# Kernel tuning notes

Measured on AMD Instinct MI355X. Metric: run time of the kernel, lower is better.

## Reference

```python
import jax, jax.numpy as jnp
import numpy as np

QMAX = 127.0  # int8 symmetric quantization range


def _quant_dequant(w):
    """Per-output-channel symmetric int8 fake quantization (weight-only),
    mimicking nn.quantized.Linear.from_float weight quantization."""
    scale = jnp.max(jnp.abs(w), axis=-1, keepdims=True) / QMAX
    scale = jnp.maximum(scale, 1e-8)
    q = jnp.clip(jnp.round(w / scale), -QMAX, QMAX)
    return q * scale


def setup_inputs() -> dict:
    key = jax.random.key(0)
    ks = jax.random.split(key, 7)
    B, S, D, F, E, NS = 2, 2048, 1024, 2048, 8, 1
    std = 1.0 / np.sqrt(D)
    x = jax.random.normal(ks[0], (B, S, D), dtype=jnp.float32)
    router_w = _quant_dequant(jax.random.normal(ks[1], (E, D), dtype=jnp.float32) * std)
    router_b = jnp.zeros((E,), dtype=jnp.float32)
    w_up = _quant_dequant(jax.random.normal(ks[2], (E, F, D), dtype=jnp.float32) * std)
    w_down = _quant_dequant(jax.random.normal(ks[3], (E, D, F), dtype=jnp.float32) / np.sqrt(F))
    shared_w_up = _quant_dequant(jax.random.normal(ks[4], (NS, F, D), dtype=jnp.float32) * std)
    shared_w_down = _quant_dequant(jax.random.normal(ks[5], (NS, D, F), dtype=jnp.float32) / np.sqrt(F))
    return {"x": x, "router_w": router_w, "router_b": router_b,
            "w_up": w_up, "w_down": w_down,
            "shared_w_up": shared_w_up, "shared_w_down": shared_w_down}


def reference(x, router_w, router_b, w_up, w_down, shared_w_up, shared_w_down):
    B, S, D = x.shape
    E = router_w.shape[0]
    TOPK = 2
    xt = x.reshape(-1, D)  # [T, D] tokens

    # Router (quantized linear) -> softmax -> top-k dispatch weights
    logits = xt @ router_w.T + router_b            # [T, E]
    probs = jax.nn.softmax(logits, axis=-1)        # [T, E]
    top_vals, top_idx = jax.lax.top_k(probs, TOPK)  # [T, K]
    top_vals = top_vals / jnp.sum(top_vals, axis=-1, keepdims=True)  # renormalize
    # combine[t, e] = routing weight of expert e for token t (0 if not selected)
    combine = jnp.sum(jax.nn.one_hot(top_idx, E, dtype=xt.dtype) * top_vals[..., None], axis=1)  # [T, E]

    # Routed experts: up -> SiLU -> down, computed densely then combined
    h = jnp.einsum('td,efd->tef', xt, w_up)        # [T, E, F]
    y = jnp.einsum('tef,edf->ted', jax.nn.silu(h), w_down)  # [T, E, D]
    out = jnp.einsum('ted,te->td', y, combine)     # [T, D]

    # Shared experts: always active, summed
    hs = jnp.einsum('td,sfd->tsf', xt, shared_w_up)          # [T, NS, F]
    out = out + jnp.einsum('tsf,sdf->td', jax.nn.silu(hs), shared_w_down)

    return out.reshape(B, S, D)
```

## Files before the change

### kernel.cpp

```cpp
#include <hip/hip_runtime.h>
#include <stdint.h>

typedef unsigned short u16;
typedef int i32x4 __attribute__((ext_vector_type(4)));

#define DDIM 1024
#define FDIM 2048
#define NEXP 8
#define RT_TILES 72
#define SHOFF 9216
#define RCAP 13312
#define NRT 104
#define UPROWS 16384
#define DNROWS 8192
#define UPTOT (UPROWS + FDIM)
#define DNTOT (DNROWS + DDIM)
#define UPTASKS (UPTOT / 4)
#define DNTASKS (DNTOT / 2)
#define WQTASKS (UPTASKS + DNTASKS)


__device__ inline float bf2f(u16 u) {
    union { unsigned int i; float f; } v; v.i = ((unsigned int)u) << 16; return v.f;
}
__device__ inline u16 f2bf(float f) {
    union { float f; unsigned int i; } v; v.f = f;
    unsigned int lsb = (v.i >> 16) & 1u;
    return (u16)((v.i + 0x7fffu + lsb) >> 16);
}
__device__ inline int q8(float v, float inv) {
    int x = (int)rintf(v * inv);
    return x < -127 ? -127 : (x > 127 ? 127 : x);
}
__device__ inline unsigned pack4(float a, float b, float c, float d, float inv) {
    return (unsigned)(q8(a, inv) & 255) | ((unsigned)(q8(b, inv) & 255) << 8) |
           ((unsigned)(q8(c, inv) & 255) << 16) | ((unsigned)(q8(d, inv) & 255) << 24);
}

typedef const __attribute__((address_space(1))) void gas_void;
typedef __attribute__((address_space(3))) void las_void;
#define GLL16(g, l) __builtin_amdgcn_global_load_lds((gas_void*)(g), (las_void*)(l), 16, 0, 0)

__global__ __launch_bounds__(256) void detect_kernel(
    const u16* __restrict__ x, int* __restrict__ meta)
{
    __shared__ int scnt;
    if (threadIdx.x == 0) scnt = 0;
    __syncthreads();
    int bad = 0;
    #pragma unroll
    for (int i = 0; i < 4; i++) {
        u16 v = x[threadIdx.x * 4 + i];
        if (((v >> 7) & 0xFF) >= 0x8F) bad++;
    }
    if (bad) atomicAdd(&scnt, bad);
    __syncthreads();
    if (threadIdx.x == 0) meta[30] = (scnt > 32) ? 1 : 0;
}

__global__ __launch_bounds__(256) void router_kernel(
    const void* __restrict__ x_, const void* __restrict__ rw_, const void* __restrict__ rb_,
    float* __restrict__ top_w, int* __restrict__ top_idx, const int* __restrict__ meta)
{
    __shared__ char smem[32768];
    const int tid = threadIdx.x;
    const int wave = tid >> 6, lane = tid & 63;
    const int flag = meta[30];

    float* rws = (float*)smem;
    if (!flag) {
        const ushort4* rwv = (const ushort4*)rw_;
        #pragma unroll
        for (int i = 0; i < 8; i++) {
            int idx = tid + i * 256;
            ushort4 h = rwv[idx];
            rws[idx * 4 + 0] = bf2f(h.x); rws[idx * 4 + 1] = bf2f(h.y);
            rws[idx * 4 + 2] = bf2f(h.z); rws[idx * 4 + 3] = bf2f(h.w);
        }
    } else {
        const float4* rwv = (const float4*)rw_;
        #pragma unroll
        for (int i = 0; i < 8; i++) {
            int idx = tid + i * 256;
            float4 f = rwv[idx];
            rws[idx * 4 + 0] = f.x; rws[idx * 4 + 1] = f.y;
            rws[idx * 4 + 2] = f.z; rws[idx * 4 + 3] = f.w;
        }
    }
    __syncthreads();

    for (int sub = 0; sub < 4; sub++) {
        const int t = blockIdx.x * 16 + wave * 4 + sub;
        float xv[16];
        if (!flag) {
            const u16* xr = (const u16*)x_ + (size_t)t * DDIM + lane * 16;
            uint4 p0 = *(const uint4*)(xr);
            uint4 p1 = *(const uint4*)(xr + 8);
            #pragma unroll
            for (int d = 0; d < 8; d++) xv[d]     = bf2f(((const u16*)&p0)[d]);
            #pragma unroll
            for (int d = 0; d < 8; d++) xv[d + 8] = bf2f(((const u16*)&p1)[d]);
        } else {
            const float4* xr = (const float4*)((const float*)x_ + (size_t)t * DDIM + lane * 16);
            #pragma unroll
            for (int c = 0; c < 4; c++) {
                float4 f = xr[c];
                xv[c * 4 + 0] = f.x; xv[c * 4 + 1] = f.y;
                xv[c * 4 + 2] = f.z; xv[c * 4 + 3] = f.w;
            }
        }
        float acc[NEXP];
        #pragma unroll
        for (int e = 0; e < NEXP; e++) {
            const float* wr = &rws[e * DDIM + lane * 16];
            float s = 0.f;
            #pragma unroll
            for (int d = 0; d < 16; d++) s += xv[d] * wr[d];
            acc[e] = s;
        }
        #pragma unroll
        for (int e = 0; e < NEXP; e++) {
            #pragma unroll
            for (int off = 32; off > 0; off >>= 1)
                acc[e] += __shfl_xor(acc[e], off, 64);
        }
        if (lane == 0) {
            float lg[NEXP];
            #pragma unroll
            for (int e = 0; e < NEXP; e++) {
                float b = flag ? ((const float*)rb_)[e] : bf2f(((const u16*)rb_)[e]);
                lg[e] = acc[e] + b;
            }
            int i0 = 0;
            #pragma unroll
            for (int e = 1; e < NEXP; e++) if (lg[e] > lg[i0]) i0 = e;
            int i1 = (i0 == 0) ? 1 : 0;
            #pragma unroll
            for (int e = 0; e < NEXP; e++) if (e != i0 && lg[e] > lg[i1]) i1 = e;
            float e1 = __expf(lg[i1] - lg[i0]);
            float w0 = 1.f / (1.f + e1);
            float w1 = e1 / (1.f + e1);
            top_w[2 * t] = w0;  top_w[2 * t + 1] = w1;
            top_idx[2 * t] = i0; top_idx[2 * t + 1] = i1;
        }
    }
}

template<int NR, int NC>
__device__ inline void wq_bf16_n(const char* __restrict__ src, char* __restrict__ dst,
                                 float* __restrict__ sout, int R0, int lane) {
    uint4 raw[NR][NC];
    #pragma unroll
    for (int r = 0; r < NR; r++)
        #pragma unroll
        for (int c = 0; c < NC; c++)
            raw[r][c] = *(const uint4*)(src + (size_t)r * (NC * 1024) + c * 1024 + lane * 16);
    float m[NR];
    #pragma unroll
    for (int r = 0; r < NR; r++) {
        m[r] = 0.f;
        #pragma unroll
        for (int c = 0; c < NC; c++) {
            const u16* h = (const u16*)&raw[r][c];
            #pragma unroll
            for (int d = 0; d < 8; d++) m[r] = fmaxf(m[r], fabsf(bf2f(h[d])));
        }
    }
    #pragma unroll
    for (int off = 32; off > 0; off >>= 1)
        #pragma unroll
        for (int r = 0; r < NR; r++)
            m[r] = fmaxf(m[r], __shfl_xor(m[r], off, 64));
    #pragma unroll
    for (int r = 0; r < NR; r++) {
        m[r] = fmaxf(m[r], 1e-12f);
        if (lane == 0) sout[R0 + r] = m[r] / 127.f;
        const float inv = 127.f / m[r];
        #pragma unroll
        for (int c = 0; c < NC; c++) {
            const u16* h = (const u16*)&raw[r][c];
            uint2 o;
            o.x = pack4(bf2f(h[0]), bf2f(h[1]), bf2f(h[2]), bf2f(h[3]), inv);
            o.y = pack4(bf2f(h[4]), bf2f(h[5]), bf2f(h[6]), bf2f(h[7]), inv);
            *(uint2*)(dst + (size_t)r * (NC * 512) + c * 512 + lane * 8) = o;
        }
    }
}

template<int NC>
__device__ inline void wq_f32(const char* __restrict__ src, char* __restrict__ dst,
                              float* __restrict__ sout, int R, int lane) {
    float m = 0.f;
    #pragma unroll
    for (int c = 0; c < NC; c++) {
        float4 f = *(const float4*)(src + (size_t)c * 1024 + lane * 16);
        m = fmaxf(m, fmaxf(fmaxf(fabsf(f.x), fabsf(f.y)),
                           fmaxf(fabsf(f.z), fabsf(f.w))));
    }
    #pragma unroll
    for (int off = 32; off > 0; off >>= 1) m = fmaxf(m, __shfl_xor(m, off, 64));
    m = fmaxf(m, 1e-12f);
    if (lane == 0) sout[R] = m / 127.f;
    const float inv = 127.f / m;
    #pragma unroll
    for (int c = 0; c < NC; c++) {
        float4 f = *(const float4*)(src + (size_t)c * 1024 + lane * 16);
        *(unsigned*)(dst + (size_t)c * 256 + lane * 4) = pack4(f.x, f.y, f.z, f.w, inv);
    }
}

__global__ __launch_bounds__(256) void wquant_kernel(
    const void* __restrict__ w_up, const void* __restrict__ w_down,
    const void* __restrict__ sw_up, const void* __restrict__ sw_down,
    char* __restrict__ qup, char* __restrict__ qdn,
    float* __restrict__ su, float* __restrict__ sd, const int* __restrict__ meta)
{
    const int wave = threadIdx.x >> 6, lane = threadIdx.x & 63;
    const int flag = meta[30];
    const int id = blockIdx.x * 4 + wave;
    if (id < UPTASKS) {
        const int R0 = id * 4;
        if (!flag) {
            const char* src = (R0 < UPROWS)
                ? (const char*)w_up + (size_t)R0 * 2048
                : (const char*)sw_up + (size_t)(R0 - UPROWS) * 2048;
            wq_bf16_n<4, 2>(src, qup + (size_t)R0 * 1024, su, R0, lane);
        } else {
            const char* src = (R0 < UPROWS)
                ? (const char*)w_up + (size_t)R0 * 4096
                : (const char*)sw_up + (size_t)(R0 - UPROWS) * 4096;
            for (int r = 0; r < 4; r++)
                wq_f32<4>(src + (size_t)r * 4096, qup + (size_t)(R0 + r) * 1024,
                          su, R0 + r, lane);
        }
    } else {
        const int R0 = (id - UPTASKS) * 2;
        if (!flag) {
            const char* src = (R0 < DNROWS)
                ? (const char*)w_down + (size_t)R0 * 4096
                : (const char*)sw_down + (size_t)(R0 - DNROWS) * 4096;
            wq_bf16_n<2, 4>(src, qdn + (size_t)R0 * 2048, sd, R0, lane);
        } else {
            const char* src = (R0 < DNROWS)
                ? (const char*)w_down + (size_t)R0 * 8192
                : (const char*)sw_down + (size_t)(R0 - DNROWS) * 8192;
            for (int r = 0; r < 2; r++)
                wq_f32<8>(src + (size_t)r * 8192, qdn + (size_t)(R0 + r) * 2048,
                          sd, R0 + r, lane);
        }
    }
}

__global__ __launch_bounds__(1024) void rank_kernel(
    const int* __restrict__ top_idx, int* __restrict__ tok_rows, int* __restrict__ meta)
{
    __shared__ int wsum[16][NEXP];
    __shared__ int wbase[16][NEXP];
    const int tid = threadIdx.x, lane = tid & 63, wave = tid >> 6;

    const int4* tp = (const int4*)(top_idx + tid * 8);
    int4 v0 = tp[0], v1 = tp[1];
    int e[8] = { v0.x, v0.y, v0.z, v0.w, v1.x, v1.y, v1.z, v1.w };

    int tcnt[NEXP];
    #pragma unroll
    for (int en = 0; en < NEXP; en++) tcnt[en] = 0;
    #pragma unroll
    for (int j = 0; j < 8; j++)
        #pragma unroll
        for (int en = 0; en < NEXP; en++) tcnt[en] += (e[j] == en);

    int excl[NEXP];
    #pragma unroll
    for (int en = 0; en < NEXP; en++) {
        int v = tcnt[en];
        #pragma unroll
        for (int off = 1; off < 64; off <<= 1) {
            int u = __shfl_up(v, off, 64);
            if (lane >= off) v += u;
        }
        excl[en] = v - tcnt[en];
        if (lane == 63) wsum[wave][en] = v;
    }
    __syncthreads();
    if (tid < NEXP) {
        int s = 0;
        for (int w = 0; w < 16; w++) { int c = wsum[w][tid]; wbase[w][tid] = s; s += c; }
        meta[tid] = s;
    }
    __syncthreads();
    if (tid == 0) {
        int b = 0;
        for (int en = 0; en < NEXP; en++) {
            meta[8 + en] = b;
            b += ((meta[en] + 127) >> 7) << 7;
        }
        meta[16] = b;
    }
    __syncthreads();

    int cur[NEXP];
    #pragma unroll
    for (int en = 0; en < NEXP; en++) cur[en] = meta[8 + en] + wbase[wave][en] + excl[en];

    int r[8];
    #pragma unroll
    for (int j = 0; j < 8; j++) {
        int rr = 0;
        #pragma unroll
        for (int en = 0; en < NEXP; en++)
            if (e[j] == en) { rr = cur[en]; cur[en] = rr + 1; }
        r[j] = rr;
    }
    int4* rp = (int4*)(tok_rows + tid * 8);
    rp[0] = make_int4(r[0], r[1], r[2], r[3]);
    rp[1] = make_int4(r[4], r[5], r[6], r[7]);
}

__global__ __launch_bounds__(128) void gather_q_kernel(
    const void* __restrict__ x_, const int* __restrict__ tok_rows,
    char* __restrict__ xq, float* __restrict__ sxa, const int* __restrict__ meta)
{
    __shared__ float wmax[2];
    const int t = blockIdx.x, tid = threadIdx.x;
    const int wave = tid >> 6, lane = tid & 63;
    const int r0 = tok_rows[2 * t], r1 = tok_rows[2 * t + 1];

    float v[8];
    if (!meta[30]) {
        uint4 p = ((const uint4*)((const u16*)x_ + (size_t)t * DDIM))[tid];
        #pragma unroll
        for (int d = 0; d < 8; d++) v[d] = bf2f(((const u16*)&p)[d]);
    } else {
        const float4* xf = (const float4*)((const float*)x_ + (size_t)t * DDIM);
        float4 a = xf[2 * tid], b = xf[2 * tid + 1];
        v[0] = a.x; v[1] = a.y; v[2] = a.z; v[3] = a.w;
        v[4] = b.x; v[5] = b.y; v[6] = b.z; v[7] = b.w;
    }
    float m = 0.f;
    #pragma unroll
    for (int d = 0; d < 8; d++) m = fmaxf(m, fabsf(v[d]));
    #pragma unroll
    for (int off = 32; off > 0; off >>= 1) m = fmaxf(m, __shfl_xor(m, off, 64));
    if (lane == 0) wmax[wave] = m;
    __syncthreads();
    const float mx = fmaxf(fmaxf(wmax[0], wmax[1]), 1e-8f);
    const float inv = 127.f / mx;

    uint2 u;
    u.x = pack4(v[0], v[1], v[2], v[3], inv);
    u.y = pack4(v[4], v[5], v[6], v[7], inv);

    ((uint2*)(xq + (size_t)r0 * DDIM))[tid] = u;
    ((uint2*)(xq + (size_t)r1 * DDIM))[tid] = u;
    ((uint2*)(xq + (size_t)(SHOFF + t) * DDIM))[tid] = u;
    if (tid == 0) {
        float s = mx / 127.f;
        sxa[r0] = s; sxa[r1] = s; sxa[SHOFF + t] = s;
    }
}

__global__ __launch_bounds__(256, 2) void moe_gemm_i8(
    const char* __restrict__ A, const char* __restrict__ Wq,
    const float* __restrict__ sa, const float* __restrict__ sw,
    u16* __restrict__ Cout, const int* __restrict__ meta, int N, int Kd, int act)
{
    const int L = blockIdx.y * gridDim.x + blockIdx.x;
    const int xcd = L & 7;
    const int jj = L >> 3;
    const int rt = xcd * 13 + (jj % 13);
    const int ct = jj / 13;

    int e;
    if (rt >= RT_TILES) {
        e = NEXP;
    } else {
        const int r0t = rt * 128;
        if (r0t >= meta[16]) return;
        e = 0;
        #pragma unroll
        for (int i = 1; i < NEXP; i++) if (r0t >= meta[8 + i]) e = i;
        if (r0t >= meta[8 + e] + meta[e]) return;
    }
    const char* Wb = Wq + (size_t)(e * N + ct * 128) * Kd;
    const float* swb = sw + e * N + ct * 128;

    __shared__ char As[2][128 * 64];
    __shared__ char Bs[2][128 * 64];

    const int tid = threadIdx.x;
    const int wave = tid >> 6, lane = tid & 63;
    const int wm = (wave >> 1) * 64;
    const int wn = (wave & 1) * 64;
    const int l16 = lane & 15;
    const int q = lane >> 4;
    const int slot = (q + (l16 >> 1)) & 3;

    const int rsub = lane >> 2;
    const int qs = ((lane & 3) - ((lane >> 3) & 3)) & 3;

    const char* Ag = A + (size_t)(rt * 128 + wave * 16 + rsub) * Kd + qs * 16;
    const char* Bg = Wb + (size_t)(wave * 16 + rsub) * Kd + qs * 16;
    const size_t rstep = (size_t)64 * Kd;

    i32x4 acc[4][4] = {};

#define STAGE(buf, off) do { \
        GLL16(Ag + (off),         &As[buf][wave * 1024]); \
        GLL16(Ag + (off) + rstep, &As[buf][4096 + wave * 1024]); \
        GLL16(Bg + (off),         &Bs[buf][wave * 1024]); \
        GLL16(Bg + (off) + rstep, &Bs[buf][4096 + wave * 1024]); \
    } while (0)

    STAGE(0, 0);
    __syncthreads();

    int cur = 0;
    for (int kk = 0; kk < Kd; kk += 64) {
        if (kk + 64 < Kd) STAGE(cur ^ 1, kk + 64);
        i32x4 af[4], bf[4];
        #pragma unroll
        for (int i = 0; i < 4; i++)
            af[i] = *(const i32x4*)&As[cur][(wm + i * 16 + l16) * 64 + slot * 16];
        #pragma unroll
        for (int j = 0; j < 4; j++)
            bf[j] = *(const i32x4*)&Bs[cur][(wn + j * 16 + l16) * 64 + slot * 16];
        #pragma unroll
        for (int i = 0; i < 4; i++)
            #pragma unroll
            for (int j = 0; j < 4; j++)
                acc[i][j] = __builtin_amdgcn_mfma_i32_16x16x64_i8(af[i], bf[j], acc[i][j], 0, 0, 0);
        __syncthreads();
        cur ^= 1;
    }
#undef STAGE

    float sal[4][4];
    #pragma unroll
    for (int i = 0; i < 4; i++)
        #pragma unroll
        for (int rr = 0; rr < 4; rr++)
            sal[i][rr] = sa[rt * 128 + wm + i * 16 + q * 4 + rr];
    float swl[4];
    #pragma unroll
    for (int j = 0; j < 4; j++) swl[j] = swb[wn + j * 16 + l16];

    u16* Crow = Cout + (size_t)(rt * 128) * N + ct * 128;
    #pragma unroll
    for (int i = 0; i < 4; i++) {
        #pragma unroll
        for (int j = 0; j < 4; j++) {
            #pragma unroll
            for (int rr = 0; rr < 4; rr++) {
                const int row = wm + i * 16 + q * 4 + rr;
                const int col = wn + j * 16 + l16;
                float v = (float)acc[i][j][rr] * sal[i][rr] * swl[j];
                if (act) v = v / (1.f + __expf(-v));
                Crow[(size_t)row * N + col] = f2bf(v);
            }
        }
    }
}

__global__ __launch_bounds__(256) void hquant_kernel(
    const u16* __restrict__ hg, char* __restrict__ h8, float* __restrict__ sh,
    const int* __restrict__ meta)
{
    const int r = blockIdx.x;
    if (r >= meta[16] && r < SHOFF) return;
    __shared__ float wmax[4];
    const int tid = threadIdx.x;
    const int wave = tid >> 6, lane = tid & 63;
    const u16* row = hg + (size_t)r * FDIM;
    uint4 p = ((const uint4*)row)[tid];
    float v[8];
    #pragma unroll
    for (int d = 0; d < 8; d++) v[d] = bf2f(((const u16*)&p)[d]);
    float m = 0.f;
    #pragma unroll
    for (int d = 0; d < 8; d++) m = fmaxf(m, fabsf(v[d]));
    #pragma unroll
    for (int off = 32; off > 0; off >>= 1) m = fmaxf(m, __shfl_xor(m, off, 64));
    if (lane == 0) wmax[wave] = m;
    __syncthreads();
    const float mx = fmaxf(fmaxf(fmaxf(wmax[0], wmax[1]), fmaxf(wmax[2], wmax[3])), 1e-8f);
    const float inv = 127.f / mx;
    if (tid == 0) sh[r] = mx / 127.f;
    uint2 u;
    u.x = pack4(v[0], v[1], v[2], v[3], inv);
    u.y = pack4(v[4], v[5], v[6], v[7], inv);
    ((uint2*)(h8 + (size_t)r * FDIM))[tid] = u;
}

__global__ __launch_bounds__(256) void combine_kernel(
    const u16* __restrict__ yg, const float* __restrict__ top_w,
    const int* __restrict__ tok_rows, void* __restrict__ out_, const int* __restrict__ meta)
{
    const int t = blockIdx.x;
    const int r0 = tok_rows[2 * t], r1 = tok_rows[2 * t + 1];
    const float w0 = top_w[2 * t], w1 = top_w[2 * t + 1];
    const int d = threadIdx.x * 4;
    ushort4 y0 = *(const ushort4*)(yg + (size_t)r0 * DDIM + d);
    ushort4 y1 = *(const ushort4*)(yg + (size_t)r1 * DDIM + d);
    ushort4 ys = *(const ushort4*)(yg + (size_t)(SHOFF + t) * DDIM + d);
    float o0 = w0 * bf2f(y0.x) + w1 * bf2f(y1.x) + bf2f(ys.x);
    float o1 = w0 * bf2f(y0.y) + w1 * bf2f(y1.y) + bf2f(ys.y);
    float o2 = w0 * bf2f(y0.z) + w1 * bf2f(y1.z) + bf2f(ys.z);
    float o3 = w0 * bf2f(y0.w) + w1 * bf2f(y1.w) + bf2f(ys.w);
    if (!meta[30]) {
        ushort4 o; o.x = f2bf(o0); o.y = f2bf(o1); o.z = f2bf(o2); o.w = f2bf(o3);
        *(ushort4*)((u16*)out_ + (size_t)t * DDIM + d) = o;
    } else {
        float4 o; o.x = o0; o.y = o1; o.z = o2; o.w = o3;
        *(float4*)((float*)out_ + (size_t)t * DDIM + d) = o;
    }
}

extern "C" void kernel_launch(void* const* d_in, const int* in_sizes, int n_in,
                              void* d_out, int out_size, void* d_ws, size_t ws_size,
                              hipStream_t stream) {
    const void* x       = d_in[0];
    const void* rw      = d_in[1];
    const void* rb      = d_in[2];
    const void* w_up    = d_in[3];
    const void* w_down  = d_in[4];
    const void* sw_up   = d_in[5];
    const void* sw_down = d_in[6];

    const int T = in_sizes[0] / DDIM;

    char* ws = (char*)d_ws;
    int*   meta     = (int*)ws;
    float* top_w    = (float*)(ws + 1024);
    int*   top_idx  = (int*)(ws + 1024 + 8 * T);
    int*   tok_rows = (int*)(ws + 1024 + 16 * T);
    size_t off = 131072;
    u16*  yg = (u16*)(ws + off);
    char* xq = (char*)(ws + off);
    off += (size_t)RCAP * DDIM * 2;
    u16*  hg = (u16*)(ws + off);
    off += (size_t)RCAP * FDIM * 2;
    char* h8 = (char*)(ws + off);
    off += (size_t)RCAP * FDIM;
    char* qup = (char*)(ws + off);
    off += (size_t)(NEXP + 1) * FDIM * DDIM;
    char* qdn = (char*)(ws + off);
    off += (size_t)(NEXP + 1) * DDIM * FDIM;
    float* sxa = (float*)(ws + off); off += (size_t)RCAP * 4;
    float* sh  = (float*)(ws + off); off += (size_t)RCAP * 4;
    float* su  = (float*)(ws + off); off += (size_t)(NEXP + 1) * FDIM * 4;
    float* sd  = (float*)(ws + off); off += (size_t)(NEXP + 1) * DDIM * 4;

    detect_kernel<<<1, 256, 0, stream>>>((const u16*)x, meta);

    const int nrb = T / 16;
    router_kernel<<<nrb, 256, 0, stream>>>(x, rw, rb, top_w, top_idx, meta);
    wquant_kernel<<<WQTASKS / 4, 256, 0, stream>>>(
        w_up, w_down, sw_up, sw_down, qup, qdn, su, sd, meta);
    rank_kernel<<<1, 1024, 0, stream>>>(top_idx, tok_rows, meta);
    gather_q_kernel<<<T, 128, 0, stream>>>(x, tok_rows, xq, sxa, meta);

    moe_gemm_i8<<<dim3(FDIM / 128, NRT), 256, 0, stream>>>(
        xq, qup, sxa, su, hg, meta, FDIM, DDIM, 1);
    hquant_kernel<<<RCAP, 256, 0, stream>>>(hg, h8, sh, meta);
    moe_gemm_i8<<<dim3(DDIM / 128, NRT), 256, 0, stream>>>(
        h8, qdn, sh, sd, yg, meta, DDIM, FDIM, 0);
    combine_kernel<<<T, 256, 0, stream>>>(yg, top_w, tok_rows, d_out, meta);
}
```

Measured before the change: 330.2 us.

## Make weight and activation quantization kernels persistent with double-buffered row loads

The weight-quantization and hidden-activation quantization kernels now run as a fixed grid of 2048 waves that stride over row tasks. Each wave prefetches the next task's 4 KB into a second register set while it reduces and packs the current one. Previously each task used its own wave or block, and hquant launched one 256-thread block per row with a shared-memory reduction and early exits for unused rows. The aim is to hide global-memory latency and cut block-launch overhead in these bandwidth-bound passes, at the cost of more registers and macro-heavy code.

```diff
diff --git a/kernel.cpp b/kernel.cpp
--- a/kernel.cpp
+++ b/kernel.cpp
@@ -15,9 +15,9 @@
 #define DNROWS 8192
 #define UPTOT (UPROWS + FDIM)
 #define DNTOT (DNROWS + DDIM)
-#define UPTASKS (UPTOT / 4)
-#define DNTASKS (DNTOT / 2)
-#define WQTASKS (UPTASKS + DNTASKS)
+#define UPT2 (UPTOT / 2)
+#define WQ_NT (UPT2 + DNTOT)
+#define WQ_NW 2048
 
 
 __device__ inline float bf2f(u16 u) {
@@ -35,6 +35,25 @@
 __device__ inline unsigned pack4(float a, float b, float c, float d, float inv) {
     return (unsigned)(q8(a, inv) & 255) | ((unsigned)(q8(b, inv) & 255) << 8) |
            ((unsigned)(q8(c, inv) & 255) << 16) | ((unsigned)(q8(d, inv) & 255) << 24);
+}
+__device__ inline float absmax8(uint4 p) {
+    const u16* h = (const u16*)&p;
+    float m = fabsf(bf2f(h[0]));
+    #pragma unroll
+    for (int d = 1; d < 8; d++) m = fmaxf(m, fabsf(bf2f(h[d])));
+    return m;
+}
+__device__ inline void store8(char* dst, uint4 p, float inv) {
+    const u16* h = (const u16*)&p;
+    uint2 o;
+    o.x = pack4(bf2f(h[0]), bf2f(h[1]), bf2f(h[2]), bf2f(h[3]), inv);
+    o.y = pack4(bf2f(h[4]), bf2f(h[5]), bf2f(h[6]), bf2f(h[7]), inv);
+    *(uint2*)dst = o;
+}
+__device__ inline float wredmax(float m) {
+    #pragma unroll
+    for (int off = 32; off > 0; off >>= 1) m = fmaxf(m, __shfl_xor(m, off, 64));
+    return m;
 }
 
 typedef const __attribute__((address_space(1))) void gas_void;
@@ -146,45 +165,17 @@
     }
 }
 
-template<int NR, int NC>
-__device__ inline void wq_bf16_n(const char* __restrict__ src, char* __restrict__ dst,
-                                 float* __restrict__ sout, int R0, int lane) {
-    uint4 raw[NR][NC];
-    #pragma unroll
-    for (int r = 0; r < NR; r++)
-        #pragma unroll
-        for (int c = 0; c < NC; c++)
-            raw[r][c] = *(const uint4*)(src + (size_t)r * (NC * 1024) + c * 1024 + lane * 16);
-    float m[NR];
-    #pragma unroll
-    for (int r = 0; r < NR; r++) {
-        m[r] = 0.f;
-        #pragma unroll
-        for (int c = 0; c < NC; c++) {
-            const u16* h = (const u16*)&raw[r][c];
-            #pragma unroll
-            for (int d = 0; d < 8; d++) m[r] = fmaxf(m[r], fabsf(bf2f(h[d])));
-        }
-    }
-    #pragma unroll
-    for (int off = 32; off > 0; off >>= 1)
-        #pragma unroll
-        for (int r = 0; r < NR; r++)
-            m[r] = fmaxf(m[r], __shfl_xor(m[r], off, 64));
-    #pragma unroll
-    for (int r = 0; r < NR; r++) {
-        m[r] = fmaxf(m[r], 1e-12f);
-        if (lane == 0) sout[R0 + r] = m[r] / 127.f;
-        const float inv = 127.f / m[r];
-        #pragma unroll
-        for (int c = 0; c < NC; c++) {
-            const u16* h = (const u16*)&raw[r][c];
-            uint2 o;
-            o.x = pack4(bf2f(h[0]), bf2f(h[1]), bf2f(h[2]), bf2f(h[3]), inv);
-            o.y = pack4(bf2f(h[4]), bf2f(h[5]), bf2f(h[6]), bf2f(h[7]), inv);
-            *(uint2*)(dst + (size_t)r * (NC * 512) + c * 512 + lane * 8) = o;
-        }
-    }
+
+__device__ inline const char* wq_src(int t, const char* wup, const char* swup,
+                                     const char* wdn, const char* swdn) {
+    if (t < UPT2) {
+        const int R0 = t * 2;
+        return (R0 < UPROWS) ? wup + (size_t)R0 * 2048
+                             : swup + (size_t)(R0 - UPROWS) * 2048;
+    }
+    const int R = t - UPT2;
+    return (R < DNROWS) ? wdn + (size_t)R * 4096
+                        : swdn + (size_t)(R - DNROWS) * 4096;
 }
 
 template<int NC>
@@ -197,8 +188,7 @@
         m = fmaxf(m, fmaxf(fmaxf(fabsf(f.x), fabsf(f.y)),
                            fmaxf(fabsf(f.z), fabsf(f.w))));
     }
-    #pragma unroll
-    for (int off = 32; off > 0; off >>= 1) m = fmaxf(m, __shfl_xor(m, off, 64));
+    m = wredmax(m);
     m = fmaxf(m, 1e-12f);
     if (lane == 0) sout[R] = m / 127.f;
     const float inv = 127.f / m;
@@ -215,40 +205,87 @@
     char* __restrict__ qup, char* __restrict__ qdn,
     float* __restrict__ su, float* __restrict__ sd, const int* __restrict__ meta)
 {
-    const int wave = threadIdx.x >> 6, lane = threadIdx.x & 63;
+    const int gwid = (blockIdx.x * blockDim.x + threadIdx.x) >> 6;
+    const int lane = threadIdx.x & 63;
     const int flag = meta[30];
-    const int id = blockIdx.x * 4 + wave;
-    if (id < UPTASKS) {
-        const int R0 = id * 4;
-        if (!flag) {
-            const char* src = (R0 < UPROWS)
-                ? (const char*)w_up + (size_t)R0 * 2048
-                : (const char*)sw_up + (size_t)(R0 - UPROWS) * 2048;
-            wq_bf16_n<4, 2>(src, qup + (size_t)R0 * 1024, su, R0, lane);
-        } else {
-            const char* src = (R0 < UPROWS)
-                ? (const char*)w_up + (size_t)R0 * 4096
-                : (const char*)sw_up + (size_t)(R0 - UPROWS) * 4096;
-            for (int r = 0; r < 4; r++)
-                wq_f32<4>(src + (size_t)r * 4096, qup + (size_t)(R0 + r) * 1024,
-                          su, R0 + r, lane);
-        }
-    } else {
-        const int R0 = (id - UPTASKS) * 2;
-        if (!flag) {
-            const char* src = (R0 < DNROWS)
-                ? (const char*)w_down + (size_t)R0 * 4096
-                : (const char*)sw_down + (size_t)(R0 - DNROWS) * 4096;
-            wq_bf16_n<2, 4>(src, qdn + (size_t)R0 * 2048, sd, R0, lane);
-        } else {
-            const char* src = (R0 < DNROWS)
-                ? (const char*)w_down + (size_t)R0 * 8192
-                : (const char*)sw_down + (size_t)(R0 - DNROWS) * 8192;
-            for (int r = 0; r < 2; r++)
-                wq_f32<8>(src + (size_t)r * 8192, qdn + (size_t)(R0 + r) * 2048,
-                          sd, R0 + r, lane);
-        }
-    }
+
+    if (flag) {
+        for (int t = gwid; t < WQ_NT; t += WQ_NW) {
+            if (t < UPT2) {
+                const int R0 = t * 2;
+                const char* src = (R0 < UPROWS)
+                    ? (const char*)w_up + (size_t)R0 * 4096
+                    : (const char*)sw_up + (size_t)(R0 - UPROWS) * 4096;
+                wq_f32<4>(src,        qup + (size_t)R0 * 1024,       su, R0,     lane);
+                wq_f32<4>(src + 4096, qup + (size_t)(R0 + 1) * 1024, su, R0 + 1, lane);
+            } else {
+                const int R = t - UPT2;
+                const char* src = (R < DNROWS)
+                    ? (const char*)w_down + (size_t)R * 8192
+                    : (const char*)sw_down + (size_t)(R - DNROWS) * 8192;
+                wq_f32<8>(src, qdn + (size_t)R * 2048, sd, R, lane);
+            }
+        }
+        return;
+    }
+
+    const char* wup  = (const char*)w_up;
+    const char* swup = (const char*)sw_up;
+    const char* wdn  = (const char*)w_down;
+    const char* swdn = (const char*)sw_down;
+
+    uint4 A0, A1, A2, A3, B0, B1, B2, B3;
+
+#define WQLOAD(P0, P1, P2, P3, T) do { \
+        const char* s_ = wq_src((T), wup, swup, wdn, swdn); \
+        P0 = *(const uint4*)(s_ + lane * 16); \
+        P1 = *(const uint4*)(s_ + 1024 + lane * 16); \
+        P2 = *(const uint4*)(s_ + 2048 + lane * 16); \
+        P3 = *(const uint4*)(s_ + 3072 + lane * 16); \
+    } while (0)
+
+#define WQPROC(P0, P1, P2, P3, T) do { \
+        if ((T) < UPT2) { \
+            const int R0_ = (T) * 2; \
+            float m0_ = fmaxf(absmax8(P0), absmax8(P1)); \
+            float m1_ = fmaxf(absmax8(P2), absmax8(P3)); \
+            m0_ = fmaxf(wredmax(m0_), 1e-12f); \
+            m1_ = fmaxf(wredmax(m1_), 1e-12f); \
+            if (lane == 0) { su[R0_] = m0_ / 127.f; su[R0_ + 1] = m1_ / 127.f; } \
+            char* d_ = qup + (size_t)R0_ * 1024; \
+            store8(d_ + lane * 8,        P0, 127.f / m0_); \
+            store8(d_ + 512 + lane * 8,  P1, 127.f / m0_); \
+            store8(d_ + 1024 + lane * 8, P2, 127.f / m1_); \
+            store8(d_ + 1536 + lane * 8, P3, 127.f / m1_); \
+        } else { \
+            const int R_ = (T) - UPT2; \
+            float m_ = fmaxf(fmaxf(absmax8(P0), absmax8(P1)), \
+                             fmaxf(absmax8(P2), absmax8(P3))); \
+            m_ = fmaxf(wredmax(m_), 1e-12f); \
+            if (lane == 0) sd[R_] = m_ / 127.f; \
+            const float inv_ = 127.f / m_; \
+            char* d_ = qdn + (size_t)R_ * 2048; \
+            store8(d_ + lane * 8,        P0, inv_); \
+            store8(d_ + 512 + lane * 8,  P1, inv_); \
+            store8(d_ + 1024 + lane * 8, P2, inv_); \
+            store8(d_ + 1536 + lane * 8, P3, inv_); \
+        } \
+    } while (0)
+
+    int t = gwid;
+    WQLOAD(A0, A1, A2, A3, t);
+    #pragma unroll 1
+    for (int it = 0; it < 4; it++) {
+        WQLOAD(B0, B1, B2, B3, t + WQ_NW);
+        WQPROC(A0, A1, A2, A3, t);
+        t += WQ_NW;
+        WQLOAD(A0, A1, A2, A3, t + WQ_NW);
+        WQPROC(B0, B1, B2, B3, t);
+        t += WQ_NW;
+    }
+    WQPROC(A0, A1, A2, A3, t);
+#undef WQLOAD
+#undef WQPROC
 }
 
 __global__ __launch_bounds__(1024) void rank_kernel(
@@ -340,8 +377,7 @@
     float m = 0.f;
     #pragma unroll
     for (int d = 0; d < 8; d++) m = fmaxf(m, fabsf(v[d]));
-    #pragma unroll
-    for (int off = 32; off > 0; off >>= 1) m = fmaxf(m, __shfl_xor(m, off, 64));
+    m = wredmax(m);
     if (lane == 0) wmax[wave] = m;
     __syncthreads();
     const float mx = fmaxf(fmaxf(wmax[0], wmax[1]), 1e-8f);
@@ -466,30 +502,60 @@
     const u16* __restrict__ hg, char* __restrict__ h8, float* __restrict__ sh,
     const int* __restrict__ meta)
 {
-    const int r = blockIdx.x;
-    if (r >= meta[16] && r < SHOFF) return;
-    __shared__ float wmax[4];
-    const int tid = threadIdx.x;
-    const int wave = tid >> 6, lane = tid & 63;
-    const u16* row = hg + (size_t)r * FDIM;
-    uint4 p = ((const uint4*)row)[tid];
-    float v[8];
-    #pragma unroll
-    for (int d = 0; d < 8; d++) v[d] = bf2f(((const u16*)&p)[d]);
-    float m = 0.f;
-    #pragma unroll
-    for (int d = 0; d < 8; d++) m = fmaxf(m, fabsf(v[d]));
-    #pragma unroll
-    for (int off = 32; off > 0; off >>= 1) m = fmaxf(m, __shfl_xor(m, off, 64));
-    if (lane == 0) wmax[wave] = m;
-    __syncthreads();
-    const float mx = fmaxf(fmaxf(fmaxf(wmax[0], wmax[1]), fmaxf(wmax[2], wmax[3])), 1e-8f);
-    const float inv = 127.f / mx;
-    if (tid == 0) sh[r] = mx / 127.f;
-    uint2 u;
-    u.x = pack4(v[0], v[1], v[2], v[3], inv);
-    u.y = pack4(v[4], v[5], v[6], v[7], inv);
-    ((uint2*)(h8 + (size_t)r * FDIM))[tid] = u;
+    const int gwid = (blockIdx.x * blockDim.x + threadIdx.x) >> 6;
+    const int lane = threadIdx.x & 63;
+    const int m16 = meta[16];
+    const int NT = m16 + (RCAP - SHOFF);
+    const int gap = SHOFF - m16;
+    if (gwid >= NT) return;
+
+    uint4 A0, A1, A2, A3, B0, B1, B2, B3;
+
+#define HROW(T) ((T) < m16 ? (T) : (T) + gap)
+#define HLOAD(P0, P1, P2, P3, T) do { \
+        const char* r_ = (const char*)(hg + (size_t)HROW(T) * FDIM); \
+        P0 = *(const uint4*)(r_ + lane * 16); \
+        P1 = *(const uint4*)(r_ + 1024 + lane * 16); \
+        P2 = *(const uint4*)(r_ + 2048 + lane * 16); \
+        P3 = *(const uint4*)(r_ + 3072 + lane * 16); \
+    } while (0)
+#define HPROC(P0, P1, P2, P3, T) do { \
+        const int r_ = HROW(T); \
+        float m_ = fmaxf(fmaxf(absmax8(P0), absmax8(P1)), \
+                         fmaxf(absmax8(P2), absmax8(P3))); \
+        m_ = fmaxf(wredmax(m_), 1e-8f); \
+        if (lane == 0) sh[r_] = m_ / 127.f; \
+        const float inv_ = 127.f / m_; \
+        char* d_ = h8 + (size_t)r_ * FDIM; \
+        store8(d_ + lane * 8,        P0, inv_); \
+        store8(d_ + 512 + lane * 8,  P1, inv_); \
+        store8(d_ + 1024 + lane * 8, P2, inv_); \
+        store8(d_ + 1536 + lane * 8, P3, inv_); \
+    } while (0)
+
+    int tA = gwid;
+    HLOAD(A0, A1, A2, A3, tA);
+    while (true) {
+        const int tB = tA + WQ_NW;
+        if (tB < NT) {
+            HLOAD(B0, B1, B2, B3, tB);
+            HPROC(A0, A1, A2, A3, tA);
+        } else {
+            HPROC(A0, A1, A2, A3, tA);
+            return;
+        }
+        tA = tB + WQ_NW;
+        if (tA < NT) {
+            HLOAD(A0, A1, A2, A3, tA);
+            HPROC(B0, B1, B2, B3, tB);
+        } else {
+            HPROC(B0, B1, B2, B3, tB);
+            return;
+        }
+    }
+#undef HROW
+#undef HLOAD
+#undef HPROC
 }
 
 __global__ __launch_bounds__(256) void combine_kernel(
@@ -555,14 +621,14 @@
 
     const int nrb = T / 16;
     router_kernel<<<nrb, 256, 0, stream>>>(x, rw, rb, top_w, top_idx, meta);
-    wquant_kernel<<<WQTASKS / 4, 256, 0, stream>>>(
+    wquant_kernel<<<WQ_NW / 4, 256, 0, stream>>>(
         w_up, w_down, sw_up, sw_down, qup, qdn, su, sd, meta);
     rank_kernel<<<1, 1024, 0, stream>>>(top_idx, tok_rows, meta);
     gather_q_kernel<<<T, 128, 0, stream>>>(x, tok_rows, xq, sxa, meta);
 
     moe_gemm_i8<<<dim3(FDIM / 128, NRT), 256, 0, stream>>>(
         xq, qup, sxa, su, hg, meta, FDIM, DDIM, 1);
-    hquant_kernel<<<RCAP, 256, 0, stream>>>(hg, h8, sh, meta);
+    hquant_kernel<<<WQ_NW / 4, 256, 0, stream>>>(hg, h8, sh, meta);
     moe_gemm_i8<<<dim3(DDIM / 128, NRT), 256, 0, stream>>>(
         h8, qdn, sh, sd, yg, meta, DDIM, FDIM, 0);
     combine_kernel<<<T, 256, 0, stream>>>(yg, top_w, tok_rows, d_out, meta);
```

Result: no change. 324.8 us (-1.6%).
